# Performance work log

Measured on AMD Instinct MI355X. Metric: run time of the kernel, lower is better.

The kernel has to match this reference:

```python
import jax, jax.numpy as jnp
import numpy as np

K = 2  # top-k experts per token


def setup_inputs() -> dict:
    key = jax.random.key(0)
    k1, k2 = jax.random.split(key)
    B, T, D, E = 4, 4096, 4096, 64
    x = jax.random.normal(k1, (B, T, D), dtype=jnp.float32)
    W = jax.random.normal(k2, (E, D), dtype=jnp.float32) * (1.0 / np.sqrt(D))
    return {"x": x, "W": W}


def reference(x, W):
    # router_logits: [B, T, E]  (nn.Linear with no bias: x @ W.T)
    router_logits = jnp.einsum('btd,ed->bte', x, W)
    # top-k over expert dim, then softmax over the k selected logits
    topk_logits, topk_idx = jax.lax.top_k(router_logits, K)  # [B,T,K]
    topk_weight = jax.nn.softmax(topk_logits, axis=-1)       # [B,T,K]
    return (topk_idx, topk_weight, router_logits)
```

## Files before the change

### kernel.cpp

```cpp
#include <hip/hip_runtime.h>
#include <math.h>

#define NTOK 16384
#define DDIM 4096
#define NEXP 64
#define TM   64
#define KC   32
#define NC   (DDIM / KC)
#define NTHR 512
#define TAU  2e-4f

typedef short bf16x8 __attribute__((ext_vector_type(8)));
typedef float f32x4  __attribute__((ext_vector_type(4)));

__device__ __forceinline__ unsigned short bf16_rne(float f) {
  unsigned u = __float_as_uint(f);
  u += 0x7fffu + ((u >> 16) & 1u);
  return (unsigned short)(u >> 16);
}

__device__ __forceinline__ void split4(float4 v, uint2& hi, uint2& lo) {
  unsigned h0 = bf16_rne(v.x), h1 = bf16_rne(v.y), h2 = bf16_rne(v.z), h3 = bf16_rne(v.w);
  float r0 = v.x - __uint_as_float(h0 << 16);
  float r1 = v.y - __uint_as_float(h1 << 16);
  float r2 = v.z - __uint_as_float(h2 << 16);
  float r3 = v.w - __uint_as_float(h3 << 16);
  unsigned l0 = bf16_rne(r0), l1 = bf16_rne(r1), l2 = bf16_rne(r2), l3 = bf16_rne(r3);
  hi = make_uint2(h0 | (h1 << 16), h2 | (h3 << 16));
  lo = make_uint2(l0 | (l1 << 16), l2 | (l3 << 16));
}

__device__ __forceinline__ bool better(float va, int ia, float vb, int ib) {
  return (va > vb) || (va == vb && ia < ib);
}
__device__ __forceinline__ bool betterd(double va, int ia, double vb, int ib) {
  return (va > vb) || (va == vb && ia < ib);
}

#define CE(va, ia, vb, ib) { if (better(vb, ib, va, ia)) { float _tv = va; va = vb; vb = _tv; int _ti = ia; ia = ib; ib = _ti; } }

__global__ __launch_bounds__(NTHR)
void topk_router_mfma(const float* __restrict__ x, const float* __restrict__ wgt,
                      float* __restrict__ out) {
  __shared__ __align__(16) short stage[2][8192];
  __shared__ __align__(16) float Lg[64][68];
  __shared__ int flagCount;
  __shared__ int flagTok[64];
  __shared__ unsigned flagIdx[64];

  const int u = threadIdx.x;
  const int l = u & 63;
  const int wid = u >> 6;
  const int wr = wid >> 1;
  const int wc = wid & 1;
  const int tokBase = blockIdx.x * TM;

  const int stok = u >> 3;
  const int skq  = u & 7;
  const int soff = (stok >> 4) * 512 + ((stok & 15) + 16 * (skq >> 1)) * 8 + (skq & 1) * 4;

  const float* xgp = x   + (size_t)(tokBase + stok) * DDIM + skq * 4;
  const float* wgp = wgt + (size_t)stok * DDIM + skq * 4;

  const int aoff  = wr * 512 + l * 8;
  const int b0off = (wc * 2) * 512 + l * 8;
  const int b1off = b0off + 512;

  f32x4 acc0 = {0.f, 0.f, 0.f, 0.f};
  f32x4 acc1 = {0.f, 0.f, 0.f, 0.f};

  if (u == 0) flagCount = 0;

  float4 xA = *(const float4*)(xgp);
  float4 wA = *(const float4*)(wgp);
  float4 xB = *(const float4*)(xgp + KC);
  float4 wB = *(const float4*)(wgp + KC);

  {
    uint2 h, lo2;
    split4(xA, h, lo2);
    *(uint2*)(&stage[0][soff]) = h;
    *(uint2*)(&stage[0][2048 + soff]) = lo2;
    split4(wA, h, lo2);
    *(uint2*)(&stage[0][4096 + soff]) = h;
    *(uint2*)(&stage[0][6144 + soff]) = lo2;
  }
  __syncthreads();

#define COMPUTE(BUF)                                                              \
  {                                                                               \
    const short* bs = &stage[BUF][0];                                             \
    bf16x8 ahi = *(const bf16x8*)(bs + aoff);                                     \
    bf16x8 alo = *(const bf16x8*)(bs + 2048 + aoff);                              \
    bf16x8 b0h = *(const bf16x8*)(bs + 4096 + b0off);                             \
    bf16x8 b0l = *(const bf16x8*)(bs + 6144 + b0off);                             \
    bf16x8 b1h = *(const bf16x8*)(bs + 4096 + b1off);                             \
    bf16x8 b1l = *(const bf16x8*)(bs + 6144 + b1off);                             \
    acc0 = __builtin_amdgcn_mfma_f32_16x16x32_bf16(ahi, b0h, acc0, 0, 0, 0);      \
    acc1 = __builtin_amdgcn_mfma_f32_16x16x32_bf16(ahi, b1h, acc1, 0, 0, 0);      \
    acc0 = __builtin_amdgcn_mfma_f32_16x16x32_bf16(ahi, b0l, acc0, 0, 0, 0);      \
    acc1 = __builtin_amdgcn_mfma_f32_16x16x32_bf16(ahi, b1l, acc1, 0, 0, 0);      \
    acc0 = __builtin_amdgcn_mfma_f32_16x16x32_bf16(alo, b0h, acc0, 0, 0, 0);      \
    acc1 = __builtin_amdgcn_mfma_f32_16x16x32_bf16(alo, b1h, acc1, 0, 0, 0);      \
  }

#define STAGEW(BUF, XV, WV)                                                       \
  {                                                                               \
    uint2 h, lo2;                                                                 \
    split4(XV, h, lo2);                                                           \
    *(uint2*)(&stage[BUF][soff]) = h;                                             \
    *(uint2*)(&stage[BUF][2048 + soff]) = lo2;                                    \
    split4(WV, h, lo2);                                                           \
    *(uint2*)(&stage[BUF][4096 + soff]) = h;                                      \
    *(uint2*)(&stage[BUF][6144 + soff]) = lo2;                                    \
  }

  for (int c = 0; c < NC; c += 2) {
    if (c + 2 < NC) { xA = *(const float4*)(xgp + (c + 2) * KC); wA = *(const float4*)(wgp + (c + 2) * KC); }
    COMPUTE(0)
    STAGEW(1, xB, wB)
    __syncthreads();
    if (c + 3 < NC) { xB = *(const float4*)(xgp + (c + 3) * KC); wB = *(const float4*)(wgp + (c + 3) * KC); }
    COMPUTE(1)
    if (c + 2 < NC) { STAGEW(0, xA, wA) }
    __syncthreads();
  }

  {
    const int trow = wr * 16 + (l >> 4) * 4;
    const int e0 = wc * 32 + (l & 15);
#pragma unroll
    for (int r = 0; r < 4; ++r) {
      Lg[trow + r][e0]      = acc0[r];
      Lg[trow + r][e0 + 16] = acc1[r];
    }
  }
  __syncthreads();

  float* out_idx = out;
  float* out_wt  = out + NTOK * 2;
  float* out_lg  = out + NTOK * 4;

  {
    const int t = u >> 3;
    const int p = u & 7;
    float4 q0 = *(const float4*)(&Lg[t][p * 8]);
    float4 q1 = *(const float4*)(&Lg[t][p * 8 + 4]);

    float* dst = out_lg + (size_t)(tokBase + t) * NEXP + p * 8;
    *(float4*)dst = q0;
    *(float4*)(dst + 4) = q1;

    int base = p * 8;
    float a0 = q0.x, a1 = q0.y, a2 = q0.z, a3 = q0.w;
    int   ia0 = base, ia1 = base + 1, ia2 = base + 2, ia3 = base + 3;
    float b0 = q1.x, b1 = q1.y, b2 = q1.z, b3 = q1.w;
    int   ib0 = base + 4, ib1 = base + 5, ib2 = base + 6, ib3 = base + 7;
    CE(a0, ia0, a1, ia1) CE(a2, ia2, a3, ia3) CE(a0, ia0, a2, ia2) CE(a1, ia1, a3, ia3) CE(a1, ia1, a2, ia2)
    CE(b0, ib0, b1, ib1) CE(b2, ib2, b3, ib3) CE(b0, ib0, b2, ib2) CE(b1, ib1, b3, ib3) CE(b1, ib1, b2, ib2)
    CE(a0, ia0, b3, ib3) CE(a1, ia1, b2, ib2) CE(a2, ia2, b1, ib1) CE(a3, ia3, b0, ib0)
    CE(a0, ia0, a2, ia2) CE(a1, ia1, a3, ia3) CE(a0, ia0, a1, ia1) CE(a2, ia2, a3, ia3)

#pragma unroll
    for (int m = 1; m <= 4; m <<= 1) {
      float b0s = __shfl_xor(a0, m); int ib0s = __shfl_xor(ia0, m);
      float b1s = __shfl_xor(a1, m); int ib1s = __shfl_xor(ia1, m);
      float b2s = __shfl_xor(a2, m); int ib2s = __shfl_xor(ia2, m);
      float b3s = __shfl_xor(a3, m); int ib3s = __shfl_xor(ia3, m);
      CE(a0, ia0, b3s, ib3s) CE(a1, ia1, b2s, ib2s) CE(a2, ia2, b1s, ib1s) CE(a3, ia3, b0s, ib0s)
      CE(a0, ia0, a2, ia2) CE(a1, ia1, a3, ia3) CE(a0, ia0, a1, ia1) CE(a2, ia2, a3, ia3)
    }

    if (p == 0) {
      const int tok = tokBase + t;
      bool flag = (a0 - a1 < TAU) || (a1 - a2 < TAU) || (a2 - a3 < TAU);
      if (!flag) {
        float ex = expf(a1 - a0);
        float den = 1.0f + ex;
        out_idx[tok * 2 + 0] = (float)ia0;
        out_idx[tok * 2 + 1] = (float)ia1;
        out_wt[tok * 2 + 0]  = 1.0f / den;
        out_wt[tok * 2 + 1]  = ex / den;
      } else {
        int pos = atomicAdd(&flagCount, 1);
        flagTok[pos] = t;
        flagIdx[pos] = (unsigned)ia0 | ((unsigned)ia1 << 8) | ((unsigned)ia2 << 16) | ((unsigned)ia3 << 24);
      }
    }
  }
  __syncthreads();

  const int nf = flagCount;
  for (int fi = wid; fi < nf; fi += 8) {
    const int t = flagTok[fi];
    const unsigned pk = flagIdx[fi];
    const int e0 = pk & 255, e1 = (pk >> 8) & 255, e2 = (pk >> 16) & 255, e3 = (pk >> 24) & 255;
    const float* xrow = x + (size_t)(tokBase + t) * DDIM + l * 64;
    const float* w0 = wgt + (size_t)e0 * DDIM + l * 64;
    const float* w1 = wgt + (size_t)e1 * DDIM + l * 64;
    const float* w2 = wgt + (size_t)e2 * DDIM + l * 64;
    const float* w3 = wgt + (size_t)e3 * DDIM + l * 64;
    double s0 = 0.0, s1 = 0.0, s2 = 0.0, s3 = 0.0;
#pragma unroll 4
    for (int j = 0; j < 64; j += 4) {
      float4 xv = *(const float4*)(xrow + j);
      float4 av = *(const float4*)(w0 + j);
      s0 = fma((double)xv.x, (double)av.x, s0); s0 = fma((double)xv.y, (double)av.y, s0);
      s0 = fma((double)xv.z, (double)av.z, s0); s0 = fma((double)xv.w, (double)av.w, s0);
      av = *(const float4*)(w1 + j);
      s1 = fma((double)xv.x, (double)av.x, s1); s1 = fma((double)xv.y, (double)av.y, s1);
      s1 = fma((double)xv.z, (double)av.z, s1); s1 = fma((double)xv.w, (double)av.w, s1);
      av = *(const float4*)(w2 + j);
      s2 = fma((double)xv.x, (double)av.x, s2); s2 = fma((double)xv.y, (double)av.y, s2);
      s2 = fma((double)xv.z, (double)av.z, s2); s2 = fma((double)xv.w, (double)av.w, s2);
      av = *(const float4*)(w3 + j);
      s3 = fma((double)xv.x, (double)av.x, s3); s3 = fma((double)xv.y, (double)av.y, s3);
      s3 = fma((double)xv.z, (double)av.z, s3); s3 = fma((double)xv.w, (double)av.w, s3);
    }
#pragma unroll
    for (int m = 1; m < 64; m <<= 1) {
      s0 += __shfl_xor(s0, m);
      s1 += __shfl_xor(s1, m);
      s2 += __shfl_xor(s2, m);
      s3 += __shfl_xor(s3, m);
    }
    if (l == 0) {
      double v0 = s0, v1 = s1, v2 = s2, v3 = s3;
      int i0 = e0, i1 = e1, i2 = e2, i3 = e3;
      if (betterd(v1, i1, v0, i0)) { double tv = v0; v0 = v1; v1 = tv; int ti = i0; i0 = i1; i1 = ti; }
      if (betterd(v3, i3, v2, i2)) { double tv = v2; v2 = v3; v3 = tv; int ti = i2; i2 = i3; i3 = ti; }
      if (betterd(v2, i2, v0, i0)) { double tv = v0; v0 = v2; v2 = tv; int ti = i0; i0 = i2; i2 = ti; }
      if (betterd(v3, i3, v1, i1)) { double tv = v1; v1 = v3; v3 = tv; int ti = i1; i1 = i3; i3 = ti; }
      if (betterd(v2, i2, v1, i1)) { double tv = v1; v1 = v2; v2 = tv; int ti = i1; i1 = i2; i2 = ti; }
      const int tok = tokBase + t;
      double ex = exp(v1 - v0);
      double den = 1.0 + ex;
      out_idx[tok * 2 + 0] = (float)i0;
      out_idx[tok * 2 + 1] = (float)i1;
      out_wt[tok * 2 + 0]  = (float)(1.0 / den);
      out_wt[tok * 2 + 1]  = (float)(ex / den);
    }
  }
}

extern "C" void kernel_launch(void* const* d_in, const int* in_sizes, int n_in,
                              void* d_out, int out_size, void* d_ws, size_t ws_size,
                              hipStream_t stream) {
  const float* x = (const float*)d_in[0];
  const float* w = (const float*)d_in[1];
  float* out = (float*)d_out;
  dim3 grid(NTOK / TM);
  dim3 block(NTHR);
  hipLaunchKernelGGL(topk_router_mfma, grid, block, 0, stream, x, w, out);
}
```

Baseline: 103.2 us.

## Presplit router weights into bf16 hi/lo MFMA layout and use LDS-free register GEMM

A separate pre-pass kernel splits W into bf16 hi/lo halves once per call and stores them in workspace in MFMA fragment order. The main kernel then drops the LDS staging and per-block barriers. Each block now handles 16 tokens with two waves, each wave covering half of D and streaming x and the pre-split weights straight into registers. A small LDS reduction combines the two halves, and the top-k runs in registers with a per-token fixup through a wave ballot. This removes the repeated W splitting and LDS traffic, at the cost of an extra launch, re-reading W fragments from L2 in every block, and lower parallelism per block.

```diff
diff --git a/kernel.cpp b/kernel.cpp
--- a/kernel.cpp
+++ b/kernel.cpp
@@ -4,11 +4,8 @@
 #define NTOK 16384
 #define DDIM 4096
 #define NEXP 64
-#define TM   64
-#define KC   32
-#define NC   (DDIM / KC)
-#define NTHR 512
 #define TAU  2e-4f
+#define WS_LO 262144
 
 typedef short bf16x8 __attribute__((ext_vector_type(8)));
 typedef float f32x4  __attribute__((ext_vector_type(4)));
@@ -30,215 +27,207 @@
   lo = make_uint2(l0 | (l1 << 16), l2 | (l3 << 16));
 }
 
+__device__ __forceinline__ bf16x8 mk8(uint2 a, uint2 b) {
+  union { uint4 u; bf16x8 v; } t;
+  t.u = make_uint4(a.x, a.y, b.x, b.y);
+  return t.v;
+}
+
 __device__ __forceinline__ bool better(float va, int ia, float vb, int ib) {
   return (va > vb) || (va == vb && ia < ib);
 }
 __device__ __forceinline__ bool betterd(double va, int ia, double vb, int ib) {
   return (va > vb) || (va == vb && ia < ib);
 }
-
 #define CE(va, ia, vb, ib) { if (better(vb, ib, va, ia)) { float _tv = va; va = vb; vb = _tv; int _ti = ia; ia = ib; ib = _ti; } }
 
-__global__ __launch_bounds__(NTHR)
-void topk_router_mfma(const float* __restrict__ x, const float* __restrict__ wgt,
-                      float* __restrict__ out) {
-  __shared__ __align__(16) short stage[2][8192];
-  __shared__ __align__(16) float Lg[64][68];
-  __shared__ int flagCount;
-  __shared__ int flagTok[64];
-  __shared__ unsigned flagIdx[64];
+__global__ __launch_bounds__(256)
+void presplit_w(const float* __restrict__ w, short* __restrict__ ws) {
+  const int tid = blockIdx.x * 256 + threadIdx.x;
+  const int e = tid >> 9;
+  const int o = tid & 511;
+  const int c = o >> 2, q = o & 3;
+  const int l = (e & 15) + 16 * q;
+  const int g = e >> 4;
+  const float* src = w + (size_t)e * DDIM + o * 8;
+  float4 v0 = *(const float4*)src;
+  float4 v1 = *(const float4*)(src + 4);
+  uint2 h0, s0, h1, s1;
+  split4(v0, h0, s0);
+  split4(v1, h1, s1);
+  const int off = c * 2048 + g * 512 + l * 8;
+  *(uint4*)(ws + off)         = make_uint4(h0.x, h0.y, h1.x, h1.y);
+  *(uint4*)(ws + WS_LO + off) = make_uint4(s0.x, s0.y, s1.x, s1.y);
+}
+
+__device__ __noinline__ void fixup_token(const float* __restrict__ x,
+                                         const float* __restrict__ wgt,
+                                         float* __restrict__ out_idx,
+                                         float* __restrict__ out_wt,
+                                         int tok, unsigned pk, int l) {
+  const int e0 = pk & 255, e1 = (pk >> 8) & 255, e2 = (pk >> 16) & 255, e3 = (pk >> 24) & 255;
+  const float* xr = x   + (size_t)tok * DDIM + l * 64;
+  const float* w0 = wgt + (size_t)e0 * DDIM + l * 64;
+  const float* w1 = wgt + (size_t)e1 * DDIM + l * 64;
+  const float* w2 = wgt + (size_t)e2 * DDIM + l * 64;
+  const float* w3 = wgt + (size_t)e3 * DDIM + l * 64;
+  double s0 = 0.0, s1 = 0.0, s2 = 0.0, s3 = 0.0;
+#pragma unroll 4
+  for (int j = 0; j < 64; j += 4) {
+    float4 xv = *(const float4*)(xr + j);
+    float4 av = *(const float4*)(w0 + j);
+    s0 = fma((double)xv.x, (double)av.x, s0); s0 = fma((double)xv.y, (double)av.y, s0);
+    s0 = fma((double)xv.z, (double)av.z, s0); s0 = fma((double)xv.w, (double)av.w, s0);
+    av = *(const float4*)(w1 + j);
+    s1 = fma((double)xv.x, (double)av.x, s1); s1 = fma((double)xv.y, (double)av.y, s1);
+    s1 = fma((double)xv.z, (double)av.z, s1); s1 = fma((double)xv.w, (double)av.w, s1);
+    av = *(const float4*)(w2 + j);
+    s2 = fma((double)xv.x, (double)av.x, s2); s2 = fma((double)xv.y, (double)av.y, s2);
+    s2 = fma((double)xv.z, (double)av.z, s2); s2 = fma((double)xv.w, (double)av.w, s2);
+    av = *(const float4*)(w3 + j);
+    s3 = fma((double)xv.x, (double)av.x, s3); s3 = fma((double)xv.y, (double)av.y, s3);
+    s3 = fma((double)xv.z, (double)av.z, s3); s3 = fma((double)xv.w, (double)av.w, s3);
+  }
+#pragma unroll
+  for (int m = 1; m < 64; m <<= 1) {
+    s0 += __shfl_xor(s0, m);
+    s1 += __shfl_xor(s1, m);
+    s2 += __shfl_xor(s2, m);
+    s3 += __shfl_xor(s3, m);
+  }
+  if (l == 0) {
+    double v0 = s0, v1 = s1, v2 = s2, v3 = s3;
+    int i0 = e0, i1 = e1, i2 = e2, i3 = e3;
+    if (betterd(v1, i1, v0, i0)) { double tv = v0; v0 = v1; v1 = tv; int ti = i0; i0 = i1; i1 = ti; }
+    if (betterd(v3, i3, v2, i2)) { double tv = v2; v2 = v3; v3 = tv; int ti = i2; i2 = i3; i3 = ti; }
+    if (betterd(v2, i2, v0, i0)) { double tv = v0; v0 = v2; v2 = tv; int ti = i0; i0 = i2; i2 = ti; }
+    if (betterd(v3, i3, v1, i1)) { double tv = v1; v1 = v3; v3 = tv; int ti = i1; i1 = i3; i3 = ti; }
+    if (betterd(v2, i2, v1, i1)) { double tv = v1; v1 = v2; v2 = tv; int ti = i1; i1 = i2; i2 = ti; }
+    double ex = exp(v1 - v0);
+    double den = 1.0 + ex;
+    out_idx[tok * 2 + 0] = (float)i0;
+    out_idx[tok * 2 + 1] = (float)i1;
+    out_wt[tok * 2 + 0]  = (float)(1.0 / den);
+    out_wt[tok * 2 + 1]  = (float)(ex / den);
+  }
+}
+
+__global__ __launch_bounds__(128, 2)
+void router_main(const float* __restrict__ x, const float* __restrict__ wgt,
+                 const short* __restrict__ ws, float* __restrict__ out) {
+  __shared__ f32x4 part[4][64];
 
   const int u = threadIdx.x;
   const int l = u & 63;
   const int wid = u >> 6;
-  const int wr = wid >> 1;
-  const int wc = wid & 1;
-  const int tokBase = blockIdx.x * TM;
-
-  const int stok = u >> 3;
-  const int skq  = u & 7;
-  const int soff = (stok >> 4) * 512 + ((stok & 15) + 16 * (skq >> 1)) * 8 + (skq & 1) * 4;
-
-  const float* xgp = x   + (size_t)(tokBase + stok) * DDIM + skq * 4;
-  const float* wgp = wgt + (size_t)stok * DDIM + skq * 4;
-
-  const int aoff  = wr * 512 + l * 8;
-  const int b0off = (wc * 2) * 512 + l * 8;
-  const int b1off = b0off + 512;
-
-  f32x4 acc0 = {0.f, 0.f, 0.f, 0.f};
-  f32x4 acc1 = {0.f, 0.f, 0.f, 0.f};
-
-  if (u == 0) flagCount = 0;
-
-  float4 xA = *(const float4*)(xgp);
-  float4 wA = *(const float4*)(wgp);
-  float4 xB = *(const float4*)(xgp + KC);
-  float4 wB = *(const float4*)(wgp + KC);
-
-  {
-    uint2 h, lo2;
-    split4(xA, h, lo2);
-    *(uint2*)(&stage[0][soff]) = h;
-    *(uint2*)(&stage[0][2048 + soff]) = lo2;
-    split4(wA, h, lo2);
-    *(uint2*)(&stage[0][4096 + soff]) = h;
-    *(uint2*)(&stage[0][6144 + soff]) = lo2;
+  const int tokBase = blockIdx.x * 16;
+
+  const float* xp = x + (size_t)(tokBase + (l & 15)) * DDIM + wid * 2048 + ((l >> 4) * 8);
+  const short* whp = ws + wid * 131072 + l * 8;
+
+  f32x4 acc[4];
+#pragma unroll
+  for (int g = 0; g < 4; ++g) acc[g] = (f32x4){0.f, 0.f, 0.f, 0.f};
+
+#define LDW(WH, WL, cc)                                                        \
+  { _Pragma("unroll")                                                          \
+    for (int g = 0; g < 4; ++g) {                                              \
+      WH[g] = *(const bf16x8*)(whp + (cc) * 2048 + g * 512);                   \
+      WL[g] = *(const bf16x8*)(whp + WS_LO + (cc) * 2048 + g * 512);           \
+    } }
+
+#define STEP(X0, X1, WH, WL, cc)                                               \
+  {                                                                            \
+    uint2 h0, s0, h1, s1;                                                      \
+    split4(X0, h0, s0);                                                        \
+    split4(X1, h1, s1);                                                        \
+    bf16x8 ahi = mk8(h0, h1);                                                  \
+    bf16x8 alo = mk8(s0, s1);                                                  \
+    if ((cc) + 4 < 64) {                                                       \
+      X0 = *(const float4*)(xp + ((cc) + 4) * 32);                             \
+      X1 = *(const float4*)(xp + ((cc) + 4) * 32 + 4);                         \
+    }                                                                          \
+    _Pragma("unroll")                                                          \
+    for (int g = 0; g < 4; ++g) {                                              \
+      acc[g] = __builtin_amdgcn_mfma_f32_16x16x32_bf16(ahi, WH[g], acc[g], 0, 0, 0); \
+      acc[g] = __builtin_amdgcn_mfma_f32_16x16x32_bf16(ahi, WL[g], acc[g], 0, 0, 0); \
+      acc[g] = __builtin_amdgcn_mfma_f32_16x16x32_bf16(alo, WH[g], acc[g], 0, 0, 0); \
+    }                                                                          \
+    if ((cc) + 2 < 64) { LDW(WH, WL, (cc) + 2) }                               \
+  }
+
+  float4 xA0 = *(const float4*)(xp + 0),  xA1 = *(const float4*)(xp + 4);
+  float4 xB0 = *(const float4*)(xp + 32), xB1 = *(const float4*)(xp + 36);
+  float4 xC0 = *(const float4*)(xp + 64), xC1 = *(const float4*)(xp + 68);
+  float4 xD0 = *(const float4*)(xp + 96), xD1 = *(const float4*)(xp + 100);
+  bf16x8 whA[4], wlA[4], whB[4], wlB[4];
+  LDW(whA, wlA, 0)
+  LDW(whB, wlB, 1)
+
+  for (int c = 0; c < 64; c += 4) {
+    STEP(xA0, xA1, whA, wlA, c)
+    STEP(xB0, xB1, whB, wlB, c + 1)
+    STEP(xC0, xC1, whA, wlA, c + 2)
+    STEP(xD0, xD1, whB, wlB, c + 3)
+  }
+
+  if (wid == 1) {
+#pragma unroll
+    for (int g = 0; g < 4; ++g) part[g][l] = acc[g];
   }
   __syncthreads();
-
-#define COMPUTE(BUF)                                                              \
-  {                                                                               \
-    const short* bs = &stage[BUF][0];                                             \
-    bf16x8 ahi = *(const bf16x8*)(bs + aoff);                                     \
-    bf16x8 alo = *(const bf16x8*)(bs + 2048 + aoff);                              \
-    bf16x8 b0h = *(const bf16x8*)(bs + 4096 + b0off);                             \
-    bf16x8 b0l = *(const bf16x8*)(bs + 6144 + b0off);                             \
-    bf16x8 b1h = *(const bf16x8*)(bs + 4096 + b1off);                             \
-    bf16x8 b1l = *(const bf16x8*)(bs + 6144 + b1off);                             \
-    acc0 = __builtin_amdgcn_mfma_f32_16x16x32_bf16(ahi, b0h, acc0, 0, 0, 0);      \
-    acc1 = __builtin_amdgcn_mfma_f32_16x16x32_bf16(ahi, b1h, acc1, 0, 0, 0);      \
-    acc0 = __builtin_amdgcn_mfma_f32_16x16x32_bf16(ahi, b0l, acc0, 0, 0, 0);      \
-    acc1 = __builtin_amdgcn_mfma_f32_16x16x32_bf16(ahi, b1l, acc1, 0, 0, 0);      \
-    acc0 = __builtin_amdgcn_mfma_f32_16x16x32_bf16(alo, b0h, acc0, 0, 0, 0);      \
-    acc1 = __builtin_amdgcn_mfma_f32_16x16x32_bf16(alo, b1h, acc1, 0, 0, 0);      \
-  }
-
-#define STAGEW(BUF, XV, WV)                                                       \
-  {                                                                               \
-    uint2 h, lo2;                                                                 \
-    split4(XV, h, lo2);                                                           \
-    *(uint2*)(&stage[BUF][soff]) = h;                                             \
-    *(uint2*)(&stage[BUF][2048 + soff]) = lo2;                                    \
-    split4(WV, h, lo2);                                                           \
-    *(uint2*)(&stage[BUF][4096 + soff]) = h;                                      \
-    *(uint2*)(&stage[BUF][6144 + soff]) = lo2;                                    \
-  }
-
-  for (int c = 0; c < NC; c += 2) {
-    if (c + 2 < NC) { xA = *(const float4*)(xgp + (c + 2) * KC); wA = *(const float4*)(wgp + (c + 2) * KC); }
-    COMPUTE(0)
-    STAGEW(1, xB, wB)
-    __syncthreads();
-    if (c + 3 < NC) { xB = *(const float4*)(xgp + (c + 3) * KC); wB = *(const float4*)(wgp + (c + 3) * KC); }
-    COMPUTE(1)
-    if (c + 2 < NC) { STAGEW(0, xA, wA) }
-    __syncthreads();
-  }
-
-  {
-    const int trow = wr * 16 + (l >> 4) * 4;
-    const int e0 = wc * 32 + (l & 15);
+  if (wid == 0) {
+#pragma unroll
+    for (int g = 0; g < 4; ++g) acc[g] += part[g][l];
+
+    float* out_idx = out;
+    float* out_wt  = out + NTOK * 2;
+    float* out_lg  = out + NTOK * 4;
+
+#pragma unroll
+    for (int g = 0; g < 4; ++g)
+#pragma unroll
+      for (int r = 0; r < 4; ++r)
+        out_lg[(size_t)(tokBase + (l >> 4) * 4 + r) * NEXP + g * 16 + (l & 15)] = acc[g][r];
+
+    const bool lead = ((l & 15) == 0);
 #pragma unroll
     for (int r = 0; r < 4; ++r) {
-      Lg[trow + r][e0]      = acc0[r];
-      Lg[trow + r][e0 + 16] = acc1[r];
-    }
-  }
-  __syncthreads();
-
-  float* out_idx = out;
-  float* out_wt  = out + NTOK * 2;
-  float* out_lg  = out + NTOK * 4;
-
-  {
-    const int t = u >> 3;
-    const int p = u & 7;
-    float4 q0 = *(const float4*)(&Lg[t][p * 8]);
-    float4 q1 = *(const float4*)(&Lg[t][p * 8 + 4]);
-
-    float* dst = out_lg + (size_t)(tokBase + t) * NEXP + p * 8;
-    *(float4*)dst = q0;
-    *(float4*)(dst + 4) = q1;
-
-    int base = p * 8;
-    float a0 = q0.x, a1 = q0.y, a2 = q0.z, a3 = q0.w;
-    int   ia0 = base, ia1 = base + 1, ia2 = base + 2, ia3 = base + 3;
-    float b0 = q1.x, b1 = q1.y, b2 = q1.z, b3 = q1.w;
-    int   ib0 = base + 4, ib1 = base + 5, ib2 = base + 6, ib3 = base + 7;
-    CE(a0, ia0, a1, ia1) CE(a2, ia2, a3, ia3) CE(a0, ia0, a2, ia2) CE(a1, ia1, a3, ia3) CE(a1, ia1, a2, ia2)
-    CE(b0, ib0, b1, ib1) CE(b2, ib2, b3, ib3) CE(b0, ib0, b2, ib2) CE(b1, ib1, b3, ib3) CE(b1, ib1, b2, ib2)
-    CE(a0, ia0, b3, ib3) CE(a1, ia1, b2, ib2) CE(a2, ia2, b1, ib1) CE(a3, ia3, b0, ib0)
-    CE(a0, ia0, a2, ia2) CE(a1, ia1, a3, ia3) CE(a0, ia0, a1, ia1) CE(a2, ia2, a3, ia3)
-
-#pragma unroll
-    for (int m = 1; m <= 4; m <<= 1) {
-      float b0s = __shfl_xor(a0, m); int ib0s = __shfl_xor(ia0, m);
-      float b1s = __shfl_xor(a1, m); int ib1s = __shfl_xor(ia1, m);
-      float b2s = __shfl_xor(a2, m); int ib2s = __shfl_xor(ia2, m);
-      float b3s = __shfl_xor(a3, m); int ib3s = __shfl_xor(ia3, m);
-      CE(a0, ia0, b3s, ib3s) CE(a1, ia1, b2s, ib2s) CE(a2, ia2, b1s, ib1s) CE(a3, ia3, b0s, ib0s)
-      CE(a0, ia0, a2, ia2) CE(a1, ia1, a3, ia3) CE(a0, ia0, a1, ia1) CE(a2, ia2, a3, ia3)
-    }
-
-    if (p == 0) {
-      const int tok = tokBase + t;
-      bool flag = (a0 - a1 < TAU) || (a1 - a2 < TAU) || (a2 - a3 < TAU);
-      if (!flag) {
-        float ex = expf(a1 - a0);
-        float den = 1.0f + ex;
-        out_idx[tok * 2 + 0] = (float)ia0;
-        out_idx[tok * 2 + 1] = (float)ia1;
-        out_wt[tok * 2 + 0]  = 1.0f / den;
-        out_wt[tok * 2 + 1]  = ex / den;
-      } else {
-        int pos = atomicAdd(&flagCount, 1);
-        flagTok[pos] = t;
-        flagIdx[pos] = (unsigned)ia0 | ((unsigned)ia1 << 8) | ((unsigned)ia2 << 16) | ((unsigned)ia3 << 24);
+      float v0 = acc[0][r], v1 = acc[1][r], v2 = acc[2][r], v3 = acc[3][r];
+      const int cbase = (l & 15);
+      int i0 = cbase, i1 = cbase + 16, i2 = cbase + 32, i3 = cbase + 48;
+      CE(v0, i0, v1, i1) CE(v2, i2, v3, i3) CE(v0, i0, v2, i2) CE(v1, i1, v3, i3) CE(v1, i1, v2, i2)
+#pragma unroll
+      for (int m = 1; m <= 8; m <<= 1) {
+        float p0 = __shfl_xor(v0, m), p1 = __shfl_xor(v1, m);
+        float p2 = __shfl_xor(v2, m), p3 = __shfl_xor(v3, m);
+        int j0 = __shfl_xor(i0, m), j1 = __shfl_xor(i1, m);
+        int j2 = __shfl_xor(i2, m), j3 = __shfl_xor(i3, m);
+        CE(v0, i0, p3, j3) CE(v1, i1, p2, j2) CE(v2, i2, p1, j1) CE(v3, i3, p0, j0)
+        CE(v0, i0, v2, i2) CE(v1, i1, v3, i3) CE(v0, i0, v1, i1) CE(v2, i2, v3, i3)
       }
-    }
-  }
-  __syncthreads();
-
-  const int nf = flagCount;
-  for (int fi = wid; fi < nf; fi += 8) {
-    const int t = flagTok[fi];
-    const unsigned pk = flagIdx[fi];
-    const int e0 = pk & 255, e1 = (pk >> 8) & 255, e2 = (pk >> 16) & 255, e3 = (pk >> 24) & 255;
-    const float* xrow = x + (size_t)(tokBase + t) * DDIM + l * 64;
-    const float* w0 = wgt + (size_t)e0 * DDIM + l * 64;
-    const float* w1 = wgt + (size_t)e1 * DDIM + l * 64;
-    const float* w2 = wgt + (size_t)e2 * DDIM + l * 64;
-    const float* w3 = wgt + (size_t)e3 * DDIM + l * 64;
-    double s0 = 0.0, s1 = 0.0, s2 = 0.0, s3 = 0.0;
-#pragma unroll 4
-    for (int j = 0; j < 64; j += 4) {
-      float4 xv = *(const float4*)(xrow + j);
-      float4 av = *(const float4*)(w0 + j);
-      s0 = fma((double)xv.x, (double)av.x, s0); s0 = fma((double)xv.y, (double)av.y, s0);
-      s0 = fma((double)xv.z, (double)av.z, s0); s0 = fma((double)xv.w, (double)av.w, s0);
-      av = *(const float4*)(w1 + j);
-      s1 = fma((double)xv.x, (double)av.x, s1); s1 = fma((double)xv.y, (double)av.y, s1);
-      s1 = fma((double)xv.z, (double)av.z, s1); s1 = fma((double)xv.w, (double)av.w, s1);
-      av = *(const float4*)(w2 + j);
-      s2 = fma((double)xv.x, (double)av.x, s2); s2 = fma((double)xv.y, (double)av.y, s2);
-      s2 = fma((double)xv.z, (double)av.z, s2); s2 = fma((double)xv.w, (double)av.w, s2);
-      av = *(const float4*)(w3 + j);
-      s3 = fma((double)xv.x, (double)av.x, s3); s3 = fma((double)xv.y, (double)av.y, s3);
-      s3 = fma((double)xv.z, (double)av.z, s3); s3 = fma((double)xv.w, (double)av.w, s3);
-    }
-#pragma unroll
-    for (int m = 1; m < 64; m <<= 1) {
-      s0 += __shfl_xor(s0, m);
-      s1 += __shfl_xor(s1, m);
-      s2 += __shfl_xor(s2, m);
-      s3 += __shfl_xor(s3, m);
-    }
-    if (l == 0) {
-      double v0 = s0, v1 = s1, v2 = s2, v3 = s3;
-      int i0 = e0, i1 = e1, i2 = e2, i3 = e3;
-      if (betterd(v1, i1, v0, i0)) { double tv = v0; v0 = v1; v1 = tv; int ti = i0; i0 = i1; i1 = ti; }
-      if (betterd(v3, i3, v2, i2)) { double tv = v2; v2 = v3; v3 = tv; int ti = i2; i2 = i3; i3 = ti; }
-      if (betterd(v2, i2, v0, i0)) { double tv = v0; v0 = v2; v2 = tv; int ti = i0; i0 = i2; i2 = ti; }
-      if (betterd(v3, i3, v1, i1)) { double tv = v1; v1 = v3; v3 = tv; int ti = i1; i1 = i3; i3 = ti; }
-      if (betterd(v2, i2, v1, i1)) { double tv = v1; v1 = v2; v2 = tv; int ti = i1; i1 = i2; i2 = ti; }
-      const int tok = tokBase + t;
-      double ex = exp(v1 - v0);
-      double den = 1.0 + ex;
-      out_idx[tok * 2 + 0] = (float)i0;
-      out_idx[tok * 2 + 1] = (float)i1;
-      out_wt[tok * 2 + 0]  = (float)(1.0 / den);
-      out_wt[tok * 2 + 1]  = (float)(ex / den);
+      bool flag = false;
+      unsigned pk = 0;
+      if (lead) {
+        flag = (v0 - v1 < TAU) || (v1 - v2 < TAU) || (v2 - v3 < TAU);
+        pk = (unsigned)i0 | ((unsigned)i1 << 8) | ((unsigned)i2 << 16) | ((unsigned)i3 << 24);
+        if (!flag) {
+          const int tok = tokBase + (l >> 4) * 4 + r;
+          float ex = expf(v1 - v0);
+          float den = 1.0f + ex;
+          out_idx[tok * 2 + 0] = (float)i0;
+          out_idx[tok * 2 + 1] = (float)i1;
+          out_wt[tok * 2 + 0]  = 1.0f / den;
+          out_wt[tok * 2 + 1]  = ex / den;
+        }
+      }
+      unsigned long long mk = __ballot(flag);
+      while (mk) {
+        const int src = __builtin_ctzll(mk);
+        mk &= mk - 1;
+        const unsigned p = (unsigned)__shfl((int)pk, src);
+        fixup_token(x, wgt, out_idx, out_wt, tokBase + (src >> 4) * 4 + r, p, l);
+      }
     }
   }
 }
@@ -249,7 +238,8 @@
   const float* x = (const float*)d_in[0];
   const float* w = (const float*)d_in[1];
   float* out = (float*)d_out;
-  dim3 grid(NTOK / TM);
-  dim3 block(NTHR);
-  hipLaunchKernelGGL(topk_router_mfma, grid, block, 0, stream, x, w, out);
-}
+  short* ws = (short*)d_ws;
+
+  hipLaunchKernelGGL(presplit_w, dim3(128), dim3(256), 0, stream, w, ws);
+  hipLaunchKernelGGL(router_main, dim3(NTOK / 16), dim3(128), 0, stream, x, w, ws, out);
+}
```

After: 107.1 us. 3.7% more time.
